# Kernel optimization log

Hardware: AMD Instinct MI355X
Metric: run time of the kernel (lower is better)

## Reference

```python
import jax, jax.numpy as jnp
import numpy as np

LAT = 512
FIN = 256
FOUT = 256
K = 3
N_STYLE = 4
B, H, W = 16, 64, 64


def setup_inputs() -> dict:
    key = jax.random.key(0)
    ks = jax.random.split(key, 8)
    x = jax.random.normal(ks[0], (B, FIN, H, W), dtype=jnp.float32)
    lat = jax.random.normal(ks[1], (B, LAT), dtype=jnp.float32)
    # main conv weight, kaiming_normal fan_in, leaky_relu a=0 -> gain sqrt(2)
    fan_in = FIN * K * K
    weight = jax.random.normal(ks[2], (FOUT, FIN, K, K), dtype=jnp.float32) * np.float32(np.sqrt(2.0 / fan_in))
    # EqualLinear layers: raw weight ~ N(0,1), runtime-scaled by 1/sqrt(in_dim)
    ws = jax.random.normal(ks[3], (N_STYLE, LAT, LAT), dtype=jnp.float32)
    bs = jnp.zeros((N_STYLE, LAT), dtype=jnp.float32)
    # final plain nn.Linear(lat_size, fin): uniform(-1/sqrt(in), 1/sqrt(in))
    bound = np.float32(1.0 / np.sqrt(LAT))
    wf = jax.random.uniform(ks[4], (FIN, LAT), dtype=jnp.float32, minval=-bound, maxval=bound)
    bf = jax.random.uniform(ks[5], (FIN,), dtype=jnp.float32, minval=-bound, maxval=bound)
    return {"x": x, "lat": lat, "weight": weight, "ws": ws, "bs": bs, "wf": wf, "bf": bf}


def reference(x, lat, weight, ws, bs, wf, bf):
    Bb, fin, Hh, Ww = x.shape
    fout, _, k, _ = weight.shape
    eq_scale = np.float32(1.0 / np.sqrt(lat.shape[1]))  # EqualLinear runtime scale

    # style MLP: n_layers_style x (EqualLinear + LeakyReLU(0.2)), then Linear -> fin
    h = lat
    for i in range(ws.shape[0]):
        h = jax.nn.leaky_relu(h @ (ws[i] * eq_scale).T + bs[i], 0.2)
    styles = h @ wf.T + bf  # [B, fin]

    # normalize base weight by inf-norm over (fin,k,k) per output channel
    wnorm = jnp.max(jnp.abs(weight), axis=(1, 2, 3), keepdims=True)
    mw = weight * (np.float32(1.0 / np.sqrt(fin * k * k)) / wnorm)  # [fout,fin,k,k]
    # normalize styles by inf-norm per sample
    styles = styles / jnp.max(jnp.abs(styles), axis=1, keepdims=True)

    # per-sample modulation + demodulation
    w = mw[None] * styles[:, None, :, None, None]  # [B,fout,fin,k,k]
    dcoefs = jax.lax.rsqrt(jnp.sum(w * w, axis=(2, 3, 4)) + 1e-8)  # [B,fout]
    w = w * dcoefs[:, :, None, None, None]
    w = w.reshape(Bb * fout, fin, k, k)

    # grouped conv with groups = batch (stride/dilation NOT passed in original -> 1)
    pad = (k - 1) // 2  # _get_same_padding with stride=1, dilation=1
    xg = x.reshape(1, Bb * fin, Hh, Ww)
    y = jax.lax.conv_general_dilated(
        xg, w, window_strides=(1, 1), padding=[(pad, pad), (pad, pad)],
        dimension_numbers=("NCHW", "OIHW", "NCHW"), feature_group_count=Bb)
    return y.reshape(Bb, fout, Hh, Ww)
```

## Files before the change

### kernel.cpp

```cpp
#include <hip/hip_runtime.h>
#include <hip/hip_bf16.h>

#define LATN 512
#define FINN 256
#define FOUTN 256
#define NB 16
#define HH 64
#define WW 64

typedef __attribute__((ext_vector_type(8))) short bf16x8;
typedef __attribute__((ext_vector_type(4))) float f32x4;
typedef __attribute__((ext_vector_type(4))) int i32x4;

#define WS_ZERO   0
#define WS_MW2    4096
#define WS_DCO    266240
#define WS_SNORM  282624
#define WS_WFMT   299008
#define WS_XM     1478656
#define WS_HA     (WS_XM)
#define WS_HB     (WS_XM + 32768)
#define WS_STY    (WS_XM + 65536)

__global__ void weight_prep_kernel(const float* __restrict__ weight,
                                   __hip_bfloat16* __restrict__ wfmt,
                                   float* __restrict__ mw2sum,
                                   float* __restrict__ zerobuf) {
    __shared__ float red[256];
    int o = blockIdx.x, t = threadIdx.x;
    if (o == 0 && t < 64) zerobuf[t] = 0.f;
    const float* wrow = weight + ((size_t)o * FINN + t) * 9;
    float wv[9];
    float mx = 0.f;
    #pragma unroll
    for (int k = 0; k < 9; ++k) { wv[k] = wrow[k]; mx = fmaxf(mx, fabsf(wv[k])); }
    red[t] = mx;
    __syncthreads();
    for (int k = 128; k > 0; k >>= 1) {
        if (t < k) red[t] = fmaxf(red[t], red[t + k]);
        __syncthreads();
    }
    float scale = (1.0f / 48.0f) / red[0];
    int obi = o >> 6, ol = o & 63, ch = t >> 5, il = t & 31;
    int slot = (il >> 3) ^ ((ol >> 1) & 3);
    char* base = (char*)wfmt + (size_t)obi * 294912 + (size_t)ch * 36864
               + (size_t)ol * 64 + slot * 16 + (il & 7) * 2;
    float s2 = 0.f;
    #pragma unroll
    for (int tap = 0; tap < 9; ++tap) {
        float m = wv[tap] * scale;
        s2 += m * m;
        *(__hip_bfloat16*)(base + tap * 4096) = __float2bfloat16(m);
    }
    mw2sum[(size_t)o * FINN + t] = s2;
}

__global__ __launch_bounds__(256) void style_layer_kernel(
    const float* __restrict__ in, const float* __restrict__ w,
    const float* __restrict__ bias, float* __restrict__ out,
    int in_dim_v4, int out_dim, float scale, int do_lrelu) {
    int t = threadIdx.x;
    int jl = t >> 4, kl = t & 15;
    int j = blockIdx.x * 16 + jl;
    int b = blockIdx.y;
    const float4* inr = (const float4*)(in + (size_t)b * (in_dim_v4 * 4));
    const float4* wr  = (const float4*)(w + (size_t)j * (in_dim_v4 * 4));
    float sum = 0.f;
    #pragma unroll 4
    for (int kb = kl; kb < in_dim_v4; kb += 16) {
        float4 wv = wr[kb], iv = inr[kb];
        sum += wv.x * iv.x + wv.y * iv.y + wv.z * iv.z + wv.w * iv.w;
    }
    #pragma unroll
    for (int off = 8; off >= 1; off >>= 1)
        sum += __shfl_xor(sum, off, 16);
    if (kl == 0) {
        float v = sum * scale + bias[j];
        if (do_lrelu && v < 0.f) v *= 0.2f;
        out[(size_t)b * out_dim + j] = v;
    }
}

__global__ __launch_bounds__(256) void norm_dcoef_kernel(
    const float* __restrict__ sty, const float* __restrict__ mw2,
    float* __restrict__ snorm, float* __restrict__ dco) {
    __shared__ float red[256];
    __shared__ float s2[256];
    int b = blockIdx.x, t = threadIdx.x;
    float v = sty[(size_t)b * FINN + t];
    red[t] = fabsf(v);
    __syncthreads();
    for (int k = 128; k > 0; k >>= 1) {
        if (t < k) red[t] = fmaxf(red[t], red[t + k]);
        __syncthreads();
    }
    float sv = v / red[0];
    snorm[(size_t)b * FINN + t] = sv;
    s2[t] = sv * sv;
    __syncthreads();
    const float4* m2 = (const float4*)(mw2 + (size_t)t * FINN);
    const float4* sq = (const float4*)s2;
    float sum = 0.f;
    #pragma unroll 8
    for (int kb = 0; kb < 64; ++kb) {
        float4 a = m2[kb], xq = sq[kb];
        sum += a.x * xq.x + a.y * xq.y + a.z * xq.z + a.w * xq.w;
    }
    dco[(size_t)b * FOUTN + t] = rsqrtf(sum + 1e-8f);
}

__global__ __launch_bounds__(256) void xcvt_kernel(const float* __restrict__ x,
                                                   const float* __restrict__ sn,
                                                   char* __restrict__ xm) {
    __shared__ float tile[64][65];
    int h = blockIdx.x, b = blockIdx.y;
    int t = threadIdx.x;
    int wl_ = t & 63, ig = t >> 6;
    char* xmb = xm + (size_t)b * 2097152;
    for (int icb = 0; icb < 4; ++icb) {
        if (icb) __syncthreads();
        #pragma unroll
        for (int p = 0; p < 16; ++p) {
            int i_l = p * 4 + ig;
            int i = icb * 64 + i_l;
            tile[i_l][wl_] = x[((size_t)(b * FINN + i)) * 4096 + h * 64 + wl_]
                             * sn[(size_t)b * FINN + i];
        }
        __syncthreads();
        #pragma unroll
        for (int rep = 0; rep < 2; ++rep) {
            int g = rep * 256 + t;
            int w = g >> 3, q8 = g & 7;
            int chunk = icb * 2 + (q8 >> 2), iq = q8 & 3;
            int slot = iq ^ (((h + 1) + ((w + 1) >> 1)) & 3);
            short tmp[8];
            #pragma unroll
            for (int j = 0; j < 8; ++j) {
                __hip_bfloat16 hb = __float2bfloat16(tile[q8 * 8 + j][w]);
                tmp[j] = *(short*)&hb;
            }
            char* dst = xmb + (size_t)chunk * 262144 + (size_t)(h * 64 + w) * 64 + slot * 16;
            *(bf16x8*)dst = *(bf16x8*)tmp;
        }
    }
}

__device__ __forceinline__ void gl_lds16(const void* g, void* l) {
    __builtin_amdgcn_global_load_lds(
        (const __attribute__((address_space(1))) unsigned int*)g,
        (__attribute__((address_space(3))) unsigned int*)l, 16, 0, 0);
}

__global__ __launch_bounds__(512, 4) void mconv_kernel(
    const char* __restrict__ xm, const char* __restrict__ wfmt,
    const float* __restrict__ dco, const float* __restrict__ zerobuf,
    float* __restrict__ y) {
    __shared__ char xs[42240];
    __shared__ char wl[36864];

    int t = threadIdx.x;
    int lane = t & 63;
    int wid = t >> 6;
    int h0 = blockIdx.x * 8;
    int obi = blockIdx.y;
    int b = blockIdx.z;

    if (t < 80) {
        int r = t >> 3, sub = t & 7;
        int col = (sub >> 2) * 65, slot = sub & 3;
        *(i32x4*)(xs + ((r * 66 + col) * 4 + slot) * 16) = (i32x4){0, 0, 0, 0};
    }

    const char* xmb = xm + (size_t)b * 2097152;
    const char* xsrc[5];
    unsigned xinc[5];
    unsigned xdst[5];
    #pragma unroll
    for (int q = 0; q < 5; ++q) {
        int idx = wid * 5 + q;
        int r = idx >> 2, quarter = idx & 3;
        int gh = h0 - 1 + r;
        bool v = (gh >= 0) && (gh < HH);
        xsrc[q] = v ? xmb + (size_t)(gh * 64 + quarter * 16) * 64 + lane * 16
                    : (const char*)zerobuf;
        xinc[q] = v ? 262144u : 0u;
        xdst[q] = (unsigned)((r * 66 + 1) * 64 + quarter * 1024);
    }
    const char* wlane = wfmt + (size_t)obi * 294912 + lane * 16;

    f32x4 acc[4][4] = {};
    int l15 = lane & 15, lg = lane >> 4;
    int wfrag = l15 * 64 + ((lg ^ ((l15 >> 1) & 3)) << 4);

    for (int ch = 0; ch < 8; ++ch) {
        if (ch) __syncthreads();
        #pragma unroll
        for (int q = 0; q < 5; ++q) {
            gl_lds16(xsrc[q], xs + xdst[q]);
            xsrc[q] += xinc[q];
        }
        #pragma unroll
        for (int q = 0; q < 5; ++q) {
            int idx = wid + q * 8;
            if (idx < 36)
                gl_lds16(wlane + idx * 1024, wl + idx * 1024);
        }
        wlane += 36864;
        __syncthreads();
        #pragma unroll
        for (int kh = 0; kh < 3; ++kh) {
            #pragma unroll
            for (int kw = 0; kw < 3; ++kw) {
                int tap = kh * 3 + kw;
                int pos0 = (wid + kh) * 66 + kw + l15;
                int xb_off = pos0 * 64 + ((lg ^ ((pos0 >> 1) & 3)) << 4);
                bf16x8 bfr[4];
                #pragma unroll
                for (int nt = 0; nt < 4; ++nt)
                    bfr[nt] = *(const bf16x8*)(xs + xb_off + nt * 1024);
                #pragma unroll
                for (int mt = 0; mt < 4; ++mt) {
                    bf16x8 af = *(const bf16x8*)(wl + tap * 4096 + mt * 1024 + wfrag);
                    #pragma unroll
                    for (int nt = 0; nt < 4; ++nt)
                        acc[mt][nt] = __builtin_amdgcn_mfma_f32_16x16x32_bf16(
                            af, bfr[nt], acc[mt][nt], 0, 0, 0);
                }
            }
        }
    }

    const float* dcb = dco + (size_t)b * FOUTN + obi * 64;
    float* yb = y + (((size_t)b * FOUTN + obi * 64) * HH + (h0 + wid)) * WW;
    #pragma unroll
    for (int mt = 0; mt < 4; ++mt) {
        #pragma unroll
        for (int j = 0; j < 4; ++j) {
            int o_l = mt * 16 + lg * 4 + j;
            float d = dcb[o_l];
            #pragma unroll
            for (int nt = 0; nt < 4; ++nt)
                yb[(size_t)o_l * 4096 + nt * 16 + l15] = acc[mt][nt][j] * d;
        }
    }
}

extern "C" void kernel_launch(void* const* d_in, const int* in_sizes, int n_in,
                              void* d_out, int out_size, void* d_ws, size_t ws_size,
                              hipStream_t stream) {
    const float* x      = (const float*)d_in[0];
    const float* lat    = (const float*)d_in[1];
    const float* weight = (const float*)d_in[2];
    const float* ws     = (const float*)d_in[3];
    const float* bs     = (const float*)d_in[4];
    const float* wf     = (const float*)d_in[5];
    const float* bf     = (const float*)d_in[6];
    float* y = (float*)d_out;

    char* base = (char*)d_ws;
    float* zerobuf = (float*)(base + WS_ZERO);
    float* mw2     = (float*)(base + WS_MW2);
    float* dco     = (float*)(base + WS_DCO);
    float* snorm   = (float*)(base + WS_SNORM);
    __hip_bfloat16* wfmt = (__hip_bfloat16*)(base + WS_WFMT);
    char* xm       = base + WS_XM;
    float* hA      = (float*)(base + WS_HA);
    float* hB      = (float*)(base + WS_HB);
    float* sty     = (float*)(base + WS_STY);

    const float eq = 0.044194173824159216f;

    weight_prep_kernel<<<FOUTN, 256, 0, stream>>>(weight, wfmt, mw2, zerobuf);
    style_layer_kernel<<<dim3(LATN / 16, NB), 256, 0, stream>>>(
        lat, ws + 0 * (size_t)LATN * LATN, bs + 0 * LATN, hA, LATN / 4, LATN, eq, 1);
    style_layer_kernel<<<dim3(LATN / 16, NB), 256, 0, stream>>>(
        hA, ws + 1 * (size_t)LATN * LATN, bs + 1 * LATN, hB, LATN / 4, LATN, eq, 1);
    style_layer_kernel<<<dim3(LATN / 16, NB), 256, 0, stream>>>(
        hB, ws + 2 * (size_t)LATN * LATN, bs + 2 * LATN, hA, LATN / 4, LATN, eq, 1);
    style_layer_kernel<<<dim3(LATN / 16, NB), 256, 0, stream>>>(
        hA, ws + 3 * (size_t)LATN * LATN, bs + 3 * LATN, hB, LATN / 4, LATN, eq, 1);
    style_layer_kernel<<<dim3(FINN / 16, NB), 256, 0, stream>>>(
        hB, wf, bf, sty, LATN / 4, FINN, 1.0f, 0);
    norm_dcoef_kernel<<<NB, 256, 0, stream>>>(sty, mw2, snorm, dco);
    xcvt_kernel<<<dim3(HH, NB), 256, 0, stream>>>(x, snorm, xm);
    mconv_kernel<<<dim3(8, 4, NB), 512, 0, stream>>>(xm, (const char*)wfmt, dco, zerobuf, y);
}
```

Before: 128.5 us.

## Fuse prep stages into one cooperative kernel and double-buffer conv LDS loads

Replaces the seven preprocessing launches (weight prep, five style MLP layers, norm/dcoef, x conversion) with a single cooperative kernel that uses grid-wide syncs between dependent stages, removing per-launch overhead and gaps. The modulated-conv kernel now double-buffers its x and weight LDS tiles, prefetching the next input-channel chunk while MFMAs run on the current one, and raises wave priority during compute. The cost is doubled LDS use, with occupancy hint lowered from 4 to 2 blocks per CU, plus grid-sync overhead and only 256 blocks doing the x conversion.

```diff
diff --git a/kernel.cpp b/kernel.cpp
--- a/kernel.cpp
+++ b/kernel.cpp
@@ -1,5 +1,8 @@
 #include <hip/hip_runtime.h>
 #include <hip/hip_bf16.h>
+#include <hip/hip_cooperative_groups.h>
+
+namespace cg = cooperative_groups;
 
 #define LATN 512
 #define FINN 256
@@ -22,125 +25,167 @@
 #define WS_HB     (WS_XM + 32768)
 #define WS_STY    (WS_XM + 65536)
 
-__global__ void weight_prep_kernel(const float* __restrict__ weight,
-                                   __hip_bfloat16* __restrict__ wfmt,
-                                   float* __restrict__ mw2sum,
-                                   float* __restrict__ zerobuf) {
+__global__ __launch_bounds__(256) void prep_kernel(
+    const float* __restrict__ x, const float* __restrict__ lat,
+    const float* __restrict__ weight, const float* __restrict__ wsm,
+    const float* __restrict__ bsm, const float* __restrict__ wf,
+    const float* __restrict__ bf,
+    __hip_bfloat16* __restrict__ wfmt, float* __restrict__ mw2,
+    float* __restrict__ snorm, float* __restrict__ dco,
+    float* __restrict__ zerobuf, char* __restrict__ xm,
+    float* __restrict__ hA, float* __restrict__ hB, float* __restrict__ sty) {
+    cg::grid_group gg = cg::this_grid();
     __shared__ float red[256];
-    int o = blockIdx.x, t = threadIdx.x;
-    if (o == 0 && t < 64) zerobuf[t] = 0.f;
-    const float* wrow = weight + ((size_t)o * FINN + t) * 9;
-    float wv[9];
-    float mx = 0.f;
-    #pragma unroll
-    for (int k = 0; k < 9; ++k) { wv[k] = wrow[k]; mx = fmaxf(mx, fabsf(wv[k])); }
-    red[t] = mx;
-    __syncthreads();
-    for (int k = 128; k > 0; k >>= 1) {
-        if (t < k) red[t] = fmaxf(red[t], red[t + k]);
-        __syncthreads();
-    }
-    float scale = (1.0f / 48.0f) / red[0];
-    int obi = o >> 6, ol = o & 63, ch = t >> 5, il = t & 31;
-    int slot = (il >> 3) ^ ((ol >> 1) & 3);
-    char* base = (char*)wfmt + (size_t)obi * 294912 + (size_t)ch * 36864
-               + (size_t)ol * 64 + slot * 16 + (il & 7) * 2;
-    float s2 = 0.f;
-    #pragma unroll
-    for (int tap = 0; tap < 9; ++tap) {
-        float m = wv[tap] * scale;
-        s2 += m * m;
-        *(__hip_bfloat16*)(base + tap * 4096) = __float2bfloat16(m);
-    }
-    mw2sum[(size_t)o * FINN + t] = s2;
-}
-
-__global__ __launch_bounds__(256) void style_layer_kernel(
-    const float* __restrict__ in, const float* __restrict__ w,
-    const float* __restrict__ bias, float* __restrict__ out,
-    int in_dim_v4, int out_dim, float scale, int do_lrelu) {
-    int t = threadIdx.x;
-    int jl = t >> 4, kl = t & 15;
-    int j = blockIdx.x * 16 + jl;
-    int b = blockIdx.y;
-    const float4* inr = (const float4*)(in + (size_t)b * (in_dim_v4 * 4));
-    const float4* wr  = (const float4*)(w + (size_t)j * (in_dim_v4 * 4));
-    float sum = 0.f;
-    #pragma unroll 4
-    for (int kb = kl; kb < in_dim_v4; kb += 16) {
-        float4 wv = wr[kb], iv = inr[kb];
-        sum += wv.x * iv.x + wv.y * iv.y + wv.z * iv.z + wv.w * iv.w;
-    }
-    #pragma unroll
-    for (int off = 8; off >= 1; off >>= 1)
-        sum += __shfl_xor(sum, off, 16);
-    if (kl == 0) {
-        float v = sum * scale + bias[j];
-        if (do_lrelu && v < 0.f) v *= 0.2f;
-        out[(size_t)b * out_dim + j] = v;
-    }
-}
-
-__global__ __launch_bounds__(256) void norm_dcoef_kernel(
-    const float* __restrict__ sty, const float* __restrict__ mw2,
-    float* __restrict__ snorm, float* __restrict__ dco) {
-    __shared__ float red[256];
-    __shared__ float s2[256];
-    int b = blockIdx.x, t = threadIdx.x;
-    float v = sty[(size_t)b * FINN + t];
-    red[t] = fabsf(v);
-    __syncthreads();
-    for (int k = 128; k > 0; k >>= 1) {
-        if (t < k) red[t] = fmaxf(red[t], red[t + k]);
-        __syncthreads();
-    }
-    float sv = v / red[0];
-    snorm[(size_t)b * FINN + t] = sv;
-    s2[t] = sv * sv;
-    __syncthreads();
-    const float4* m2 = (const float4*)(mw2 + (size_t)t * FINN);
-    const float4* sq = (const float4*)s2;
-    float sum = 0.f;
-    #pragma unroll 8
-    for (int kb = 0; kb < 64; ++kb) {
-        float4 a = m2[kb], xq = sq[kb];
-        sum += a.x * xq.x + a.y * xq.y + a.z * xq.z + a.w * xq.w;
-    }
-    dco[(size_t)b * FOUTN + t] = rsqrtf(sum + 1e-8f);
-}
-
-__global__ __launch_bounds__(256) void xcvt_kernel(const float* __restrict__ x,
-                                                   const float* __restrict__ sn,
-                                                   char* __restrict__ xm) {
+    __shared__ float lin[512];
     __shared__ float tile[64][65];
-    int h = blockIdx.x, b = blockIdx.y;
-    int t = threadIdx.x;
-    int wl_ = t & 63, ig = t >> 6;
-    char* xmb = xm + (size_t)b * 2097152;
-    for (int icb = 0; icb < 4; ++icb) {
-        if (icb) __syncthreads();
-        #pragma unroll
-        for (int p = 0; p < 16; ++p) {
-            int i_l = p * 4 + ig;
-            int i = icb * 64 + i_l;
-            tile[i_l][wl_] = x[((size_t)(b * FINN + i)) * 4096 + h * 64 + wl_]
-                             * sn[(size_t)b * FINN + i];
-        }
-        __syncthreads();
-        #pragma unroll
-        for (int rep = 0; rep < 2; ++rep) {
-            int g = rep * 256 + t;
-            int w = g >> 3, q8 = g & 7;
-            int chunk = icb * 2 + (q8 >> 2), iq = q8 & 3;
-            int slot = iq ^ (((h + 1) + ((w + 1) >> 1)) & 3);
-            short tmp[8];
-            #pragma unroll
-            for (int j = 0; j < 8; ++j) {
-                __hip_bfloat16 hb = __float2bfloat16(tile[q8 * 8 + j][w]);
-                tmp[j] = *(short*)&hb;
-            }
-            char* dst = xmb + (size_t)chunk * 262144 + (size_t)(h * 64 + w) * 64 + slot * 16;
-            *(bf16x8*)dst = *(bf16x8*)tmp;
+    int bi = blockIdx.x, t = threadIdx.x;
+
+    {
+        int o = bi;
+        if (o == 0 && t < 64) zerobuf[t] = 0.f;
+        const float* wrow = weight + ((size_t)o * FINN + t) * 9;
+        float wv[9];
+        float mx = 0.f;
+        #pragma unroll
+        for (int k = 0; k < 9; ++k) { wv[k] = wrow[k]; mx = fmaxf(mx, fabsf(wv[k])); }
+        red[t] = mx;
+        __syncthreads();
+        for (int k = 128; k > 0; k >>= 1) {
+            if (t < k) red[t] = fmaxf(red[t], red[t + k]);
+            __syncthreads();
+        }
+        float scale = (1.0f / 48.0f) / red[0];
+        int obi = o >> 6, ol = o & 63, ch = t >> 5, il = t & 31;
+        int slot = (il >> 3) ^ ((ol >> 1) & 3);
+        char* basep = (char*)wfmt + (size_t)obi * 294912 + (size_t)ch * 36864
+                    + (size_t)ol * 64 + slot * 16 + (il & 7) * 2;
+        float s2 = 0.f;
+        #pragma unroll
+        for (int tap = 0; tap < 9; ++tap) {
+            float m = wv[tap] * scale;
+            s2 += m * m;
+            *(__hip_bfloat16*)(basep + tap * 4096) = __float2bfloat16(m);
+        }
+        mw2[(size_t)o * FINN + t] = s2;
+    }
+
+    const float eq = 0.044194173824159216f;
+    {
+        int b = bi & 15, j0 = (bi >> 4) * 32;
+        const float* in = lat;
+        float* out = hA;
+        for (int l = 0; l < 4; ++l) {
+            __syncthreads();
+            lin[t] = in[(size_t)b * 512 + t];
+            lin[t + 256] = in[(size_t)b * 512 + 256 + t];
+            __syncthreads();
+            int jl = t >> 3, kl = t & 7;
+            int j = j0 + jl;
+            const float4* wr = (const float4*)(wsm + (size_t)l * 262144 + (size_t)j * 512);
+            const float4* iv = (const float4*)lin;
+            float sum = 0.f;
+            #pragma unroll 4
+            for (int kb = kl; kb < 128; kb += 8) {
+                float4 wv = wr[kb], vv = iv[kb];
+                sum += wv.x * vv.x + wv.y * vv.y + wv.z * vv.z + wv.w * vv.w;
+            }
+            sum += __shfl_xor(sum, 1, 8);
+            sum += __shfl_xor(sum, 2, 8);
+            sum += __shfl_xor(sum, 4, 8);
+            if (kl == 0) {
+                float v = sum * eq + bsm[l * 512 + j];
+                out[(size_t)b * 512 + j] = (v < 0.f) ? 0.2f * v : v;
+            }
+            gg.sync();
+            in = out;
+            out = (l & 1) ? hA : hB;
+        }
+    }
+    {
+        int b = bi & 15, j0 = (bi >> 4) * 16;
+        lin[t] = hB[(size_t)b * 512 + t];
+        lin[t + 256] = hB[(size_t)b * 512 + 256 + t];
+        __syncthreads();
+        int jl = t >> 4, kl = t & 15;
+        int j = j0 + jl;
+        const float4* wr = (const float4*)(wf + (size_t)j * 512);
+        const float4* iv = (const float4*)lin;
+        float sum = 0.f;
+        #pragma unroll 4
+        for (int kb = kl; kb < 128; kb += 16) {
+            float4 wv = wr[kb], vv = iv[kb];
+            sum += wv.x * vv.x + wv.y * vv.y + wv.z * vv.z + wv.w * vv.w;
+        }
+        #pragma unroll
+        for (int off = 8; off >= 1; off >>= 1) sum += __shfl_xor(sum, off, 16);
+        if (kl == 0) sty[(size_t)b * 256 + j] = sum + bf[j];
+    }
+    gg.sync();
+    if (bi < 16) {
+        int b = bi;
+        float v = sty[(size_t)b * 256 + t];
+        red[t] = fabsf(v);
+        __syncthreads();
+        for (int k = 128; k > 0; k >>= 1) {
+            if (t < k) red[t] = fmaxf(red[t], red[t + k]);
+            __syncthreads();
+        }
+        snorm[(size_t)b * 256 + t] = v / red[0];
+    }
+    gg.sync();
+    {
+        int b = bi & 15, o0 = (bi >> 4) * 16;
+        float sv = snorm[(size_t)b * 256 + t];
+        __syncthreads();
+        lin[t] = sv * sv;
+        __syncthreads();
+        int ol = t >> 4, kl = t & 15;
+        int o = o0 + ol;
+        const float4* m2 = (const float4*)(mw2 + (size_t)o * 256);
+        const float4* sq = (const float4*)lin;
+        float sum = 0.f;
+        #pragma unroll
+        for (int kb = kl; kb < 64; kb += 16) {
+            float4 a = m2[kb], xq = sq[kb];
+            sum += a.x * xq.x + a.y * xq.y + a.z * xq.z + a.w * xq.w;
+        }
+        #pragma unroll
+        for (int off = 8; off >= 1; off >>= 1) sum += __shfl_xor(sum, off, 16);
+        if (kl == 0) dco[(size_t)b * 256 + o] = rsqrtf(sum + 1e-8f);
+    }
+    {
+        int wl_ = t & 63, ig = t >> 6;
+        for (int s = 0; s < 4; ++s) {
+            int id = bi * 4 + s;
+            int b = id >> 6, h = id & 63;
+            char* xmb = xm + (size_t)b * 2097152;
+            for (int icb = 0; icb < 4; ++icb) {
+                __syncthreads();
+                #pragma unroll
+                for (int p = 0; p < 16; ++p) {
+                    int i_l = p * 4 + ig;
+                    int i = icb * 64 + i_l;
+                    tile[i_l][wl_] = x[((size_t)(b * FINN + i)) * 4096 + h * 64 + wl_]
+                                     * snorm[(size_t)b * FINN + i];
+                }
+                __syncthreads();
+                #pragma unroll
+                for (int rep = 0; rep < 2; ++rep) {
+                    int g = rep * 256 + t;
+                    int w = g >> 3, q8 = g & 7;
+                    int chunk = icb * 2 + (q8 >> 2), iq = q8 & 3;
+                    int slot = iq ^ (((h + 1) + ((w + 1) >> 1)) & 3);
+                    short tmp[8];
+                    #pragma unroll
+                    for (int j = 0; j < 8; ++j) {
+                        __hip_bfloat16 hb = __float2bfloat16(tile[q8 * 8 + j][w]);
+                        tmp[j] = *(short*)&hb;
+                    }
+                    char* dst = xmb + (size_t)chunk * 262144
+                              + (size_t)(h * 64 + w) * 64 + slot * 16;
+                    *(bf16x8*)dst = *(bf16x8*)tmp;
+                }
+            }
         }
     }
 }
@@ -151,12 +196,12 @@
         (__attribute__((address_space(3))) unsigned int*)l, 16, 0, 0);
 }
 
-__global__ __launch_bounds__(512, 4) void mconv_kernel(
+__global__ __launch_bounds__(512, 2) void mconv_kernel(
     const char* __restrict__ xm, const char* __restrict__ wfmt,
     const float* __restrict__ dco, const float* __restrict__ zerobuf,
     float* __restrict__ y) {
-    __shared__ char xs[42240];
-    __shared__ char wl[36864];
+    __shared__ char xs[2][42240];
+    __shared__ char wl[2][36864];
 
     int t = threadIdx.x;
     int lane = t & 63;
@@ -165,10 +210,11 @@
     int obi = blockIdx.y;
     int b = blockIdx.z;
 
-    if (t < 80) {
-        int r = t >> 3, sub = t & 7;
+    if (t < 160) {
+        int bufi = t / 80, u = t % 80;
+        int r = u >> 3, sub = u & 7;
         int col = (sub >> 2) * 65, slot = sub & 3;
-        *(i32x4*)(xs + ((r * 66 + col) * 4 + slot) * 16) = (i32x4){0, 0, 0, 0};
+        *(i32x4*)(xs[bufi] + ((r * 66 + col) * 4 + slot) * 16) = (i32x4){0, 0, 0, 0};
     }
 
     const char* xmb = xm + (size_t)b * 2097152;
@@ -192,21 +238,39 @@
     int l15 = lane & 15, lg = lane >> 4;
     int wfrag = l15 * 64 + ((lg ^ ((l15 >> 1) & 3)) << 4);
 
+    #pragma unroll
+    for (int q = 0; q < 5; ++q) {
+        gl_lds16(xsrc[q], xs[0] + xdst[q]);
+        xsrc[q] += xinc[q];
+    }
+    #pragma unroll
+    for (int q = 0; q < 5; ++q) {
+        int idx = wid + q * 8;
+        if (idx < 36) gl_lds16(wlane + idx * 1024, wl[0] + idx * 1024);
+    }
+    wlane += 36864;
+    asm volatile("s_waitcnt vmcnt(0)" ::: "memory");
+    __builtin_amdgcn_s_barrier();
+    __builtin_amdgcn_sched_barrier(0);
+
     for (int ch = 0; ch < 8; ++ch) {
-        if (ch) __syncthreads();
-        #pragma unroll
-        for (int q = 0; q < 5; ++q) {
-            gl_lds16(xsrc[q], xs + xdst[q]);
-            xsrc[q] += xinc[q];
-        }
-        #pragma unroll
-        for (int q = 0; q < 5; ++q) {
-            int idx = wid + q * 8;
-            if (idx < 36)
-                gl_lds16(wlane + idx * 1024, wl + idx * 1024);
-        }
-        wlane += 36864;
-        __syncthreads();
+        int cur = ch & 1;
+        if (ch < 7) {
+            #pragma unroll
+            for (int q = 0; q < 5; ++q) {
+                gl_lds16(xsrc[q], xs[cur ^ 1] + xdst[q]);
+                xsrc[q] += xinc[q];
+            }
+            #pragma unroll
+            for (int q = 0; q < 5; ++q) {
+                int idx = wid + q * 8;
+                if (idx < 36) gl_lds16(wlane + idx * 1024, wl[cur ^ 1] + idx * 1024);
+            }
+            wlane += 36864;
+        }
+        const char* xsb = xs[cur];
+        const char* wlb = wl[cur];
+        __builtin_amdgcn_s_setprio(1);
         #pragma unroll
         for (int kh = 0; kh < 3; ++kh) {
             #pragma unroll
@@ -217,10 +281,10 @@
                 bf16x8 bfr[4];
                 #pragma unroll
                 for (int nt = 0; nt < 4; ++nt)
-                    bfr[nt] = *(const bf16x8*)(xs + xb_off + nt * 1024);
+                    bfr[nt] = *(const bf16x8*)(xsb + xb_off + nt * 1024);
                 #pragma unroll
                 for (int mt = 0; mt < 4; ++mt) {
-                    bf16x8 af = *(const bf16x8*)(wl + tap * 4096 + mt * 1024 + wfrag);
+                    bf16x8 af = *(const bf16x8*)(wlb + tap * 4096 + mt * 1024 + wfrag);
                     #pragma unroll
                     for (int nt = 0; nt < 4; ++nt)
                         acc[mt][nt] = __builtin_amdgcn_mfma_f32_16x16x32_bf16(
@@ -228,6 +292,10 @@
                 }
             }
         }
+        __builtin_amdgcn_s_setprio(0);
+        asm volatile("s_waitcnt vmcnt(0)" ::: "memory");
+        __builtin_amdgcn_s_barrier();
+        __builtin_amdgcn_sched_barrier(0);
     }
 
     const float* dcb = dco + (size_t)b * FOUTN + obi * 64;
@@ -251,10 +319,10 @@
     const float* x      = (const float*)d_in[0];
     const float* lat    = (const float*)d_in[1];
     const float* weight = (const float*)d_in[2];
-    const float* ws     = (const float*)d_in[3];
-    const float* bs     = (const float*)d_in[4];
-    const float* wf     = (const float*)d_in[5];
-    const float* bf     = (const float*)d_in[6];
+    const float* wsm    = (const float*)d_in[3];
+    const float* bsm    = (const float*)d_in[4];
+    const float* wff    = (const float*)d_in[5];
+    const float* bff    = (const float*)d_in[6];
     float* y = (float*)d_out;
 
     char* base = (char*)d_ws;
@@ -268,20 +336,11 @@
     float* hB      = (float*)(base + WS_HB);
     float* sty     = (float*)(base + WS_STY);
 
-    const float eq = 0.044194173824159216f;
-
-    weight_prep_kernel<<<FOUTN, 256, 0, stream>>>(weight, wfmt, mw2, zerobuf);
-    style_layer_kernel<<<dim3(LATN / 16, NB), 256, 0, stream>>>(
-        lat, ws + 0 * (size_t)LATN * LATN, bs + 0 * LATN, hA, LATN / 4, LATN, eq, 1);
-    style_layer_kernel<<<dim3(LATN / 16, NB), 256, 0, stream>>>(
-        hA, ws + 1 * (size_t)LATN * LATN, bs + 1 * LATN, hB, LATN / 4, LATN, eq, 1);
-    style_layer_kernel<<<dim3(LATN / 16, NB), 256, 0, stream>>>(
-        hB, ws + 2 * (size_t)LATN * LATN, bs + 2 * LATN, hA, LATN / 4, LATN, eq, 1);
-    style_layer_kernel<<<dim3(LATN / 16, NB), 256, 0, stream>>>(
-        hA, ws + 3 * (size_t)LATN * LATN, bs + 3 * LATN, hB, LATN / 4, LATN, eq, 1);
-    style_layer_kernel<<<dim3(FINN / 16, NB), 256, 0, stream>>>(
-        hB, wf, bf, sty, LATN / 4, FINN, 1.0f, 0);
-    norm_dcoef_kernel<<<NB, 256, 0, stream>>>(sty, mw2, snorm, dco);
-    xcvt_kernel<<<dim3(HH, NB), 256, 0, stream>>>(x, snorm, xm);
+    void* args[] = {
+        (void*)&x, (void*)&lat, (void*)&weight, (void*)&wsm, (void*)&bsm,
+        (void*)&wff, (void*)&bff, (void*)&wfmt, (void*)&mw2, (void*)&snorm,
+        (void*)&dco, (void*)&zerobuf, (void*)&xm, (void*)&hA, (void*)&hB, (void*)&sty
+    };
+    hipLaunchCooperativeKernel((void*)prep_kernel, dim3(256), dim3(256), args, 0, stream);
     mconv_kernel<<<dim3(8, 4, NB), 512, 0, stream>>>(xm, (const char*)wfmt, dco, zerobuf, y);
 }
```

Result: slower. 325.2 us (+153.0%).

## Double-buffer LDS tiles in modulated conv to overlap loads with MFMA

Applied to the files above, without the earlier changes.

The conv kernel's LDS input and weight tiles become two buffers, so the next channel chunk is fetched with global_load_lds while MFMAs run on the current chunk. The two __syncthreads per chunk are replaced by one s_waitcnt plus barrier at the end of each iteration, and wave priority is raised during the MFMA section. LDS use per block roughly doubles (about 158KB), which lowers the launch bound from 4 to 2 and reduces resident blocks per CU. Some variables are renamed along the way.

```diff
diff --git a/kernel.cpp b/kernel.cpp
--- a/kernel.cpp
+++ b/kernel.cpp
@@ -43,14 +43,14 @@
     float scale = (1.0f / 48.0f) / red[0];
     int obi = o >> 6, ol = o & 63, ch = t >> 5, il = t & 31;
     int slot = (il >> 3) ^ ((ol >> 1) & 3);
-    char* base = (char*)wfmt + (size_t)obi * 294912 + (size_t)ch * 36864
-               + (size_t)ol * 64 + slot * 16 + (il & 7) * 2;
+    char* basep = (char*)wfmt + (size_t)obi * 294912 + (size_t)ch * 36864
+                + (size_t)ol * 64 + slot * 16 + (il & 7) * 2;
     float s2 = 0.f;
     #pragma unroll
     for (int tap = 0; tap < 9; ++tap) {
         float m = wv[tap] * scale;
         s2 += m * m;
-        *(__hip_bfloat16*)(base + tap * 4096) = __float2bfloat16(m);
+        *(__hip_bfloat16*)(basep + tap * 4096) = __float2bfloat16(m);
     }
     mw2sum[(size_t)o * FINN + t] = s2;
 }
@@ -151,12 +151,12 @@
         (__attribute__((address_space(3))) unsigned int*)l, 16, 0, 0);
 }
 
-__global__ __launch_bounds__(512, 4) void mconv_kernel(
+__global__ __launch_bounds__(512, 2) void mconv_kernel(
     const char* __restrict__ xm, const char* __restrict__ wfmt,
     const float* __restrict__ dco, const float* __restrict__ zerobuf,
     float* __restrict__ y) {
-    __shared__ char xs[42240];
-    __shared__ char wl[36864];
+    __shared__ char xs[2][42240];
+    __shared__ char wl[2][36864];
 
     int t = threadIdx.x;
     int lane = t & 63;
@@ -165,10 +165,11 @@
     int obi = blockIdx.y;
     int b = blockIdx.z;
 
-    if (t < 80) {
-        int r = t >> 3, sub = t & 7;
+    if (t < 160) {
+        int bufi = t / 80, u = t % 80;
+        int r = u >> 3, sub = u & 7;
         int col = (sub >> 2) * 65, slot = sub & 3;
-        *(i32x4*)(xs + ((r * 66 + col) * 4 + slot) * 16) = (i32x4){0, 0, 0, 0};
+        *(i32x4*)(xs[bufi] + ((r * 66 + col) * 4 + slot) * 16) = (i32x4){0, 0, 0, 0};
     }
 
     const char* xmb = xm + (size_t)b * 2097152;
@@ -192,21 +193,39 @@
     int l15 = lane & 15, lg = lane >> 4;
     int wfrag = l15 * 64 + ((lg ^ ((l15 >> 1) & 3)) << 4);
 
+    #pragma unroll
+    for (int q = 0; q < 5; ++q) {
+        gl_lds16(xsrc[q], xs[0] + xdst[q]);
+        xsrc[q] += xinc[q];
+    }
+    #pragma unroll
+    for (int q = 0; q < 5; ++q) {
+        int idx = wid + q * 8;
+        if (idx < 36) gl_lds16(wlane + idx * 1024, wl[0] + idx * 1024);
+    }
+    wlane += 36864;
+    asm volatile("s_waitcnt vmcnt(0)" ::: "memory");
+    __builtin_amdgcn_s_barrier();
+    __builtin_amdgcn_sched_barrier(0);
+
     for (int ch = 0; ch < 8; ++ch) {
-        if (ch) __syncthreads();
-        #pragma unroll
-        for (int q = 0; q < 5; ++q) {
-            gl_lds16(xsrc[q], xs + xdst[q]);
-            xsrc[q] += xinc[q];
-        }
-        #pragma unroll
-        for (int q = 0; q < 5; ++q) {
-            int idx = wid + q * 8;
-            if (idx < 36)
-                gl_lds16(wlane + idx * 1024, wl + idx * 1024);
-        }
-        wlane += 36864;
-        __syncthreads();
+        int cur = ch & 1;
+        if (ch < 7) {
+            #pragma unroll
+            for (int q = 0; q < 5; ++q) {
+                gl_lds16(xsrc[q], xs[cur ^ 1] + xdst[q]);
+                xsrc[q] += xinc[q];
+            }
+            #pragma unroll
+            for (int q = 0; q < 5; ++q) {
+                int idx = wid + q * 8;
+                if (idx < 36) gl_lds16(wlane + idx * 1024, wl[cur ^ 1] + idx * 1024);
+            }
+            wlane += 36864;
+        }
+        const char* xsb = xs[cur];
+        const char* wlb = wl[cur];
+        __builtin_amdgcn_s_setprio(1);
         #pragma unroll
         for (int kh = 0; kh < 3; ++kh) {
             #pragma unroll
@@ -217,10 +236,10 @@
                 bf16x8 bfr[4];
                 #pragma unroll
                 for (int nt = 0; nt < 4; ++nt)
-                    bfr[nt] = *(const bf16x8*)(xs + xb_off + nt * 1024);
+                    bfr[nt] = *(const bf16x8*)(xsb + xb_off + nt * 1024);
                 #pragma unroll
                 for (int mt = 0; mt < 4; ++mt) {
-                    bf16x8 af = *(const bf16x8*)(wl + tap * 4096 + mt * 1024 + wfrag);
+                    bf16x8 af = *(const bf16x8*)(wlb + tap * 4096 + mt * 1024 + wfrag);
                     #pragma unroll
                     for (int nt = 0; nt < 4; ++nt)
                         acc[mt][nt] = __builtin_amdgcn_mfma_f32_16x16x32_bf16(
@@ -228,6 +247,10 @@
                 }
             }
         }
+        __builtin_amdgcn_s_setprio(0);
+        asm volatile("s_waitcnt vmcnt(0)" ::: "memory");
+        __builtin_amdgcn_s_barrier();
+        __builtin_amdgcn_sched_barrier(0);
     }
 
     const float* dcb = dco + (size_t)b * FOUTN + obi * 64;
@@ -251,10 +274,10 @@
     const float* x      = (const float*)d_in[0];
     const float* lat    = (const float*)d_in[1];
     const float* weight = (const float*)d_in[2];
-    const float* ws     = (const float*)d_in[3];
-    const float* bs     = (const float*)d_in[4];
-    const float* wf     = (const float*)d_in[5];
-    const float* bf     = (const float*)d_in[6];
+    const float* wsm    = (const float*)d_in[3];
+    const float* bsm    = (const float*)d_in[4];
+    const float* wff    = (const float*)d_in[5];
+    const float* bff    = (const float*)d_in[6];
     float* y = (float*)d_out;
 
     char* base = (char*)d_ws;
@@ -272,15 +295,15 @@
 
     weight_prep_kernel<<<FOUTN, 256, 0, stream>>>(weight, wfmt, mw2, zerobuf);
     style_layer_kernel<<<dim3(LATN / 16, NB), 256, 0, stream>>>(
-        lat, ws + 0 * (size_t)LATN * LATN, bs + 0 * LATN, hA, LATN / 4, LATN, eq, 1);
+        lat, wsm + 0 * (size_t)LATN * LATN, bsm + 0 * LATN, hA, LATN / 4, LATN, eq, 1);
     style_layer_kernel<<<dim3(LATN / 16, NB), 256, 0, stream>>>(
-        hA, ws + 1 * (size_t)LATN * LATN, bs + 1 * LATN, hB, LATN / 4, LATN, eq, 1);
+        hA, wsm + 1 * (size_t)LATN * LATN, bsm + 1 * LATN, hB, LATN / 4, LATN, eq, 1);
     style_layer_kernel<<<dim3(LATN / 16, NB), 256, 0, stream>>>(
-        hB, ws + 2 * (size_t)LATN * LATN, bs + 2 * LATN, hA, LATN / 4, LATN, eq, 1);
+        hB, wsm + 2 * (size_t)LATN * LATN, bsm + 2 * LATN, hA, LATN / 4, LATN, eq, 1);
     style_layer_kernel<<<dim3(LATN / 16, NB), 256, 0, stream>>>(
-        hA, ws + 3 * (size_t)LATN * LATN, bs + 3 * LATN, hB, LATN / 4, LATN, eq, 1);
+        hA, wsm + 3 * (size_t)LATN * LATN, bsm + 3 * LATN, hB, LATN / 4, LATN, eq, 1);
     style_layer_kernel<<<dim3(FINN / 16, NB), 256, 0, stream>>>(
-        hB, wf, bf, sty, LATN / 4, FINN, 1.0f, 0);
+        hB, wff, bff, sty, LATN / 4, FINN, 1.0f, 0);
     norm_dcoef_kernel<<<NB, 256, 0, stream>>>(sty, mw2, snorm, dco);
     xcvt_kernel<<<dim3(HH, NB), 256, 0, stream>>>(x, snorm, xm);
     mconv_kernel<<<dim3(8, 4, NB), 512, 0, stream>>>(xm, (const char*)wfmt, dco, zerobuf, y);
```

Result: faster. 119.3 us (-7.2%).
